# Kernel tuning notes

Hardware: AMD Instinct MI355X
Metric: run time of the kernel (lower is better)

Reference implementation:

```python
import jax, jax.numpy as jnp
import numpy as np

B, S, H = 2, 2048, 2048
NH, NKV, HD = 16, 4, 128
ROPE_BASE = 10000.0


def setup_inputs() -> dict:
    key = jax.random.key(0)
    ks = jax.random.split(key, 5)
    x = jax.random.normal(ks[0], (B, S, H), dtype=jnp.float32)
    position_ids = jnp.arange(S, dtype=jnp.int64 if jax.config.jax_enable_x64 else jnp.int32).reshape(1, S)
    # Linear weights stored as [in, out] (equivalent to torch weight.T)
    sc = 1.0 / np.sqrt(H)
    Wq = jax.random.normal(ks[1], (H, NH * HD), dtype=jnp.float32) * sc
    Wk = jax.random.normal(ks[2], (H, NKV * HD), dtype=jnp.float32) * sc
    Wv = jax.random.normal(ks[3], (H, NKV * HD), dtype=jnp.float32) * sc
    Wo = jax.random.normal(ks[4], (NH * HD, H), dtype=jnp.float32) * (1.0 / np.sqrt(NH * HD))
    return {"x": x, "position_ids": position_ids, "Wq": Wq, "Wk": Wk, "Wv": Wv, "Wo": Wo}


def _rope(q, k, position_ids):
    # q: [B,S,NH,HD], k: [B,S,NKV,HD]; Llama-style half-split RoPE
    half = HD // 2
    inv_freq = 1.0 / (ROPE_BASE ** (jnp.arange(0, half, dtype=jnp.float32) * 2.0 / HD))
    ang = position_ids.astype(jnp.float32)[..., None] * inv_freq  # [b,S,half]
    cos = jnp.concatenate([jnp.cos(ang), jnp.cos(ang)], axis=-1)[:, :, None, :]  # [b,S,1,HD]
    sin = jnp.concatenate([jnp.sin(ang), jnp.sin(ang)], axis=-1)[:, :, None, :]

    def rot_half(t):
        t1, t2 = t[..., :half], t[..., half:]
        return jnp.concatenate([-t2, t1], axis=-1)

    return q * cos + rot_half(q) * sin, k * cos + rot_half(k) * sin


def reference(x, position_ids, Wq, Wk, Wv, Wo):
    b, s, _ = x.shape
    q = (x @ Wq).reshape(b, s, NH, HD)
    k = (x @ Wk).reshape(b, s, NKV, HD)
    v = (x @ Wv).reshape(b, s, NKV, HD)
    q, k = _rope(q, k, position_ids)
    reps = NH // NKV
    k = jnp.repeat(k, reps, axis=2)  # repeat_interleave on head dim
    v = jnp.repeat(v, reps, axis=2)
    q = q.transpose(0, 2, 1, 3)  # [b,h,s,d]
    k = k.transpose(0, 2, 1, 3)
    v = v.transpose(0, 2, 1, 3)
    scores = jnp.einsum('bhqd,bhkd->bhqk', q, k) / jnp.sqrt(jnp.float32(HD))
    causal = jnp.triu(jnp.ones((s, s), dtype=bool), k=1)
    scores = jnp.where(causal, -jnp.inf, scores)
    attn = jax.nn.softmax(scores.astype(jnp.float32), axis=-1).astype(q.dtype)
    out = jnp.einsum('bhqk,bhkd->bhqd', attn, v)
    out = out.transpose(0, 2, 1, 3).reshape(b, s, NH * HD)
    return out @ Wo
```

## Files before the change

### kernel.cpp

```cpp
#include <hip/hip_runtime.h>
#include <stdint.h>

typedef unsigned short u16;
typedef __attribute__((ext_vector_type(8))) short short8;
typedef __attribute__((ext_vector_type(4))) float floatx4;

#define S_LEN 2048
#define NQKV 3072

#if __has_builtin(__builtin_amdgcn_exp2f)
#define EXP2F __builtin_amdgcn_exp2f
#else
#define EXP2F exp2f
#endif

__device__ inline float bf2f(u16 u) {
  union { uint32_t u; float f; } v; v.u = ((uint32_t)u) << 16; return v.f;
}
__device__ inline u16 f2bf(float f) {
  union { float f; uint32_t u; } v; v.f = f;
  uint32_t r = v.u + 0x7fffu + ((v.u >> 16) & 1u);
  return (u16)(r >> 16);
}
__device__ inline void gl2lds16(const u16* g, u16* l) {
  __builtin_amdgcn_global_load_lds((const __attribute__((address_space(1))) uint32_t*)g,
                                   (__attribute__((address_space(3))) uint32_t*)l, 16, 0, 0);
}

__global__ void cast_k(const float* __restrict__ in, u16* __restrict__ out, int n4) {
  int i = blockIdx.x * 256 + threadIdx.x;
  if (i >= n4) return;
  float4 v = ((const float4*)in)[i];
  ushort4 o;
  o.x = f2bf(v.x); o.y = f2bf(v.y); o.z = f2bf(v.z); o.w = f2bf(v.w);
  ((ushort4*)out)[i] = o;
}

__global__ void transpose_k(const float* __restrict__ in, u16* __restrict__ out, int K, int N) {
  __shared__ u16 tile[32][33];
  int n0 = blockIdx.x * 32, k0 = blockIdx.y * 32;
  int tx = threadIdx.x, ty = threadIdx.y;
#pragma unroll
  for (int i = 0; i < 4; i++)
    tile[ty + 8 * i][tx] = f2bf(in[(size_t)(k0 + ty + 8 * i) * N + n0 + tx]);
  __syncthreads();
#pragma unroll
  for (int i = 0; i < 4; i++)
    out[(size_t)(n0 + ty + 8 * i) * K + k0 + tx] = tile[tx][ty + 8 * i];
}

__global__ void vtrans_k(const u16* __restrict__ qkv, u16* __restrict__ vt) {
  __shared__ u16 tile[32][33];
  int bk = blockIdx.x * 32, bd = blockIdx.y * 32, bz = blockIdx.z;
  int bb = bz >> 2, kvh = bz & 3;
  const u16* src = qkv + ((size_t)bb * S_LEN) * NQKV + 2560 + kvh * 128;
  u16* dst = vt + (size_t)bz * 128 * 2048;
  int tx = threadIdx.x, ty = threadIdx.y;
#pragma unroll
  for (int i = 0; i < 4; i++)
    tile[ty + 8 * i][tx] = src[(size_t)(bk + ty + 8 * i) * NQKV + bd + tx];
  __syncthreads();
#pragma unroll
  for (int i = 0; i < 4; i++)
    dst[(size_t)(bd + ty + 8 * i) * 2048 + bk + tx] = tile[tx][ty + 8 * i];
}

template <bool OUTF32>
__global__ __launch_bounds__(256) void gemm_bt(const u16* __restrict__ A, const u16* __restrict__ Bt,
                                               void* __restrict__ Cv, int M, int N, int K) {
  __shared__ u16 As[128 * 32];
  __shared__ u16 Bs[128 * 32];
  const int m0 = blockIdx.y * 128, n0 = blockIdx.x * 128;
  const int t = threadIdx.x, w = t >> 6, lane = t & 63;
  const int quad = lane >> 4, l16 = lane & 15;
  const int wm = (w >> 1) * 64, wn = (w & 1) * 64;
  const int lrow = lane >> 2, lk = (lane & 3) * 8;
  floatx4 acc[4][4] = {};
  for (int k0 = 0; k0 < K; k0 += 32) {
#pragma unroll
    for (int c = 2 * w; c <= 2 * w + 1; ++c) {
      int row = c * 16 + lrow;
      gl2lds16(A + (size_t)(m0 + row) * K + k0 + lk, As + c * 512 + lane * 8);
      gl2lds16(Bt + (size_t)(n0 + row) * K + k0 + lk, Bs + c * 512 + lane * 8);
    }
    __syncthreads();
    short8 a[4], b[4];
#pragma unroll
    for (int mt = 0; mt < 4; mt++) a[mt] = *(const short8*)(As + (wm + mt * 16 + l16) * 32 + quad * 8);
#pragma unroll
    for (int nt = 0; nt < 4; nt++) b[nt] = *(const short8*)(Bs + (wn + nt * 16 + l16) * 32 + quad * 8);
#pragma unroll
    for (int mt = 0; mt < 4; mt++)
#pragma unroll
      for (int nt = 0; nt < 4; nt++)
        acc[mt][nt] = __builtin_amdgcn_mfma_f32_16x16x32_bf16(a[mt], b[nt], acc[mt][nt], 0, 0, 0);
    __syncthreads();
  }
#pragma unroll
  for (int mt = 0; mt < 4; mt++)
#pragma unroll
    for (int nt = 0; nt < 4; nt++)
#pragma unroll
      for (int r = 0; r < 4; r++) {
        int row = m0 + wm + mt * 16 + quad * 4 + r;
        int col = n0 + wn + nt * 16 + l16;
        if (OUTF32)
          ((float*)Cv)[(size_t)row * N + col] = acc[mt][nt][r];
        else
          ((u16*)Cv)[(size_t)row * N + col] = f2bf(acc[mt][nt][r]);
      }
}

__global__ __launch_bounds__(512, 2) void gemm256_k(const u16* __restrict__ A,
                                                    const u16* __restrict__ Bt,
                                                    u16* __restrict__ C, int N, int K) {
  __shared__ u16 Al[2][2][8192];
  __shared__ u16 Bl[2][2][8192];
  const int TN = N >> 8;
  int flat = blockIdx.x;
  const int cpx = gridDim.x >> 3;
  flat = (flat & 7) * cpx + (flat >> 3);
  const int m0 = (flat / TN) << 8, n0 = (flat % TN) << 8;
  const int t = threadIdx.x, w = t >> 6, lane = t & 63;
  const int quad = lane >> 4, l16 = lane & 15;
  const int wm = w >> 2, wn = w & 3;
  const int sr = t >> 3, sl = t & 7;
  floatx4 acc[2][2][4][2] = {};
  const int NKT = K >> 6;

  const int ra_l = wm * 64 + l16;
  const int rb_l = wn * 32 + l16;

#pragma unroll
  for (int round = 0; round < 2; round++) {
    int r = round * 64 + sr;
    int so = (sl ^ (r & 7)) << 3;
    gl2lds16(A + (size_t)(m0 + r) * K + so, &Al[0][0][0] + round * 4096 + t * 8);
    gl2lds16(Bt + (size_t)(n0 + r) * K + so, &Bl[0][0][0] + round * 4096 + t * 8);
    gl2lds16(Bt + (size_t)(n0 + 128 + r) * K + so, &Bl[0][1][0] + round * 4096 + t * 8);
    gl2lds16(A + (size_t)(m0 + 128 + r) * K + so, &Al[0][1][0] + round * 4096 + t * 8);
  }
  asm volatile("s_waitcnt vmcnt(0)" ::: "memory");
  __builtin_amdgcn_s_barrier();

  short8 af[4][2];
  short8 bf[2][2][2];

  for (int kt = 0; kt < NKT; kt++) {
    const int c = kt & 1;
    const u16* Ab = &Al[c][0][0];
    const u16* Bb = &Bl[c][0][0];
    u16* An = &Al[c ^ 1][0][0];
    u16* Bn = &Bl[c ^ 1][0][0];
    const int k1 = (kt + 1) << 6;
    const bool pf = (kt + 1 < NKT);
#pragma unroll
    for (int ph = 0; ph < 4; ph++) {
      const int mh = (ph >> 1);
      const int nh = (ph == 1 || ph == 2) ? 1 : 0;
      if (ph == 0 || ph == 2) {
#pragma unroll
        for (int mt = 0; mt < 4; mt++) {
          int ra = ra_l + mt * 16;
          const u16* base = Ab + mh * 8192 + ra * 64;
#pragma unroll
          for (int ks = 0; ks < 2; ks++)
            af[mt][ks] = *(const short8*)(base + (((ks * 4 + quad) ^ (ra & 7)) << 3));
        }
      }
      if (ph == 0 || ph == 1) {
#pragma unroll
        for (int nt = 0; nt < 2; nt++) {
          int rb = rb_l + nt * 16;
          const u16* base = Bb + nh * 8192 + rb * 64;
#pragma unroll
          for (int ks = 0; ks < 2; ks++)
            bf[nh][nt][ks] = *(const short8*)(base + (((ks * 4 + quad) ^ (rb & 7)) << 3));
        }
      }
      if (pf) {
        const u16* G;
        u16* L;
        int rbase;
        if (ph == 0)      { G = A;  L = An;        rbase = m0; }
        else if (ph == 1) { G = Bt; L = Bn;        rbase = n0; }
        else if (ph == 2) { G = Bt; L = Bn + 8192; rbase = n0 + 128; }
        else              { G = A;  L = An + 8192; rbase = m0 + 128; }
#pragma unroll
        for (int round = 0; round < 2; round++) {
          int r = round * 64 + sr;
          gl2lds16(G + (size_t)(rbase + r) * K + k1 + ((sl ^ (r & 7)) << 3),
                   L + round * 4096 + t * 8);
        }
      }
      __builtin_amdgcn_s_barrier();
      asm volatile("s_waitcnt lgkmcnt(0)" ::: "memory");
      __builtin_amdgcn_s_setprio(1);
#pragma unroll
      for (int mt = 0; mt < 4; mt++)
#pragma unroll
        for (int nt = 0; nt < 2; nt++)
#pragma unroll
          for (int ks = 0; ks < 2; ks++)
            acc[mh][nh][mt][nt] =
                __builtin_amdgcn_mfma_f32_16x16x32_bf16(af[mt][ks], bf[nh][nt][ks], acc[mh][nh][mt][nt], 0, 0, 0);
      __builtin_amdgcn_s_setprio(0);
      if (ph != 2) asm volatile("s_waitcnt vmcnt(4)" ::: "memory");
      __builtin_amdgcn_s_barrier();
    }
  }
#pragma unroll
  for (int mh = 0; mh < 2; mh++)
#pragma unroll
    for (int nh = 0; nh < 2; nh++)
#pragma unroll
      for (int mt = 0; mt < 4; mt++)
#pragma unroll
        for (int nt = 0; nt < 2; nt++)
#pragma unroll
          for (int r = 0; r < 4; r++) {
            int row = m0 + mh * 128 + wm * 64 + mt * 16 + quad * 4 + r;
            int col = n0 + nh * 128 + wn * 32 + nt * 16 + l16;
            C[(size_t)row * N + col] = f2bf(acc[mh][nh][mt][nt][r]);
          }
}

__global__ void rope_k(u16* __restrict__ qkv, const int* __restrict__ pos) {
  int idx = blockIdx.x * 256 + threadIdx.x;
  int i = idx & 63;
  int hh = (idx >> 6) % 20;
  int row = idx / (64 * 20);
  int s = row & (S_LEN - 1);
  float p = (float)pos[s];
  float freq = __expf(-(float)i * 0.015625f * 9.210340371976184f);
  float ang = p * freq;
  float c = cosf(ang), sn = sinf(ang);
  int col = (hh < 16) ? hh * 128 : 2048 + (hh - 16) * 128;
  size_t base = (size_t)row * NQKV + col + i;
  float t1 = bf2f(qkv[base]), t2 = bf2f(qkv[base + 64]);
  qkv[base] = f2bf(t1 * c - t2 * sn);
  qkv[base + 64] = f2bf(t2 * c + t1 * sn);
}

#define PL_LD 72
__global__ __launch_bounds__(256) void attn_k(const u16* __restrict__ qkv,
                                              const u16* __restrict__ vt,
                                              u16* __restrict__ ctx) {
  __shared__ u16 Kl[2][64 * 128];
  __shared__ u16 Vl[2][128 * 64];
  __shared__ u16 Pl[4][16 * PL_LD];
  const int p = blockIdx.x;
  const int h = blockIdx.y, bb = blockIdx.z;
  const int kvh = h >> 2;
  const int t = threadIdx.x, w = t >> 6, lane = t & 63;
  const int quad = lane >> 4, l16 = lane & 15;
  const int sx = l16 & 7;
  const int kkey0 = w * 16 + (lane >> 4);
  const int kslot = lane & 15;
  const int vd0 = w * 32 + (lane >> 3);
  const int vslot = lane & 7;
  const size_t rowbase = (size_t)bb * S_LEN;
  const u16* Kg0 = qkv + rowbase * NQKV + 2048 + kvh * 128;
  const u16* Vg0 = vt + (size_t)(bb * 4 + kvh) * 128 * 2048;
  const float c2 = 0.12751744f;
  short8 onesf = {16256, 16256, 16256, 16256, 16256, 16256, 16256, 16256};

  for (int phase = 0; phase < 2; phase++) {
    const int qt = phase ? p : 31 - p;
    const int rw = qt * 64 + w * 16;

    short8 qf[4];
#pragma unroll
    for (int ks = 0; ks < 4; ks++)
      qf[ks] = *(const short8*)(qkv + (rowbase + rw + l16) * NQKV + h * 128 + ks * 32 + quad * 8);

    floatx4 acc[8] = {};
    floatx4 accl = {0.f, 0.f, 0.f, 0.f};

    __syncthreads();
    {
      const u16* Kg = Kg0;
      const u16* Vg = Vg0;
#pragma unroll
      for (int ii = 0; ii < 4; ii++) {
        int key = kkey0 + ii * 4;
        gl2lds16(Kg + (size_t)key * NQKV + ((kslot ^ (key & 7)) * 8),
                 &Kl[0][0] + w * 2048 + ii * 512 + lane * 8);
      }
#pragma unroll
      for (int ii = 0; ii < 4; ii++) {
        int d = vd0 + ii * 8;
        gl2lds16(Vg + (size_t)d * 2048 + ((vslot ^ (d & 7)) * 8),
                 &Vl[0][0] + w * 2048 + ii * 512 + lane * 8);
      }
    }

    for (int kb = 0; kb <= qt; kb++) {
      const int cur = kb & 1;
      __syncthreads();
      if (kb < qt) {
        const u16* Kg = Kg0 + (size_t)(kb + 1) * 64 * NQKV;
        const u16* Vg = Vg0 + (kb + 1) * 64;
        u16* KlN = &Kl[cur ^ 1][0];
        u16* VlN = &Vl[cur ^ 1][0];
#pragma unroll
        for (int ii = 0; ii < 4; ii++) {
          int key = kkey0 + ii * 4;
          gl2lds16(Kg + (size_t)key * NQKV + ((kslot ^ (key & 7)) * 8),
                   KlN + w * 2048 + ii * 512 + lane * 8);
        }
#pragma unroll
        for (int ii = 0; ii < 4; ii++) {
          int d = vd0 + ii * 8;
          gl2lds16(Vg + (size_t)d * 2048 + ((vslot ^ (d & 7)) * 8),
                   VlN + w * 2048 + ii * 512 + lane * 8);
        }
      }
      const u16* KlB = &Kl[cur][0];
      const u16* VlB = &Vl[cur][0];

      floatx4 sc[4];
#pragma unroll
      for (int nt = 0; nt < 4; nt++) {
        const u16* Krow = KlB + (nt * 16 + l16) * 128;
        short8 kf[4];
#pragma unroll
        for (int ks = 0; ks < 4; ks++)
          kf[ks] = *(const short8*)(Krow + (((ks * 4 + quad) ^ sx) * 8));
        floatx4 s = {0.f, 0.f, 0.f, 0.f};
#pragma unroll
        for (int ks = 0; ks < 4; ks++) s = __builtin_amdgcn_mfma_f32_16x16x32_bf16(qf[ks], kf[ks], s, 0, 0, 0);
        sc[nt] = s;
      }
      const bool diag = (kb == qt);
#pragma unroll
      for (int nt = 0; nt < 4; nt++)
#pragma unroll
        for (int r = 0; r < 4; r++) {
          float e = EXP2F(sc[nt][r] * c2);
          if (diag) {
            int keyg = kb * 64 + nt * 16 + l16;
            int rowg = rw + quad * 4 + r;
            if (keyg > rowg) e = 0.f;
          }
          Pl[w][(quad * 4 + r) * PL_LD + nt * 16 + l16] = (u16)(__float_as_uint(e) >> 16);
        }
      short8 pf[2];
#pragma unroll
      for (int kh = 0; kh < 2; kh++)
        pf[kh] = *(const short8*)(&Pl[w][0] + l16 * PL_LD + kh * 32 + quad * 8);
      accl = __builtin_amdgcn_mfma_f32_16x16x32_bf16(pf[0], onesf, accl, 0, 0, 0);
      accl = __builtin_amdgcn_mfma_f32_16x16x32_bf16(pf[1], onesf, accl, 0, 0, 0);
#pragma unroll
      for (int nto = 0; nto < 8; nto++) {
        const u16* Vrow = VlB + (nto * 16 + l16) * 64;
        short8 vf0 = *(const short8*)(Vrow + ((quad ^ sx) * 8));
        short8 vf1 = *(const short8*)(Vrow + (((quad + 4) ^ sx) * 8));
        acc[nto] = __builtin_amdgcn_mfma_f32_16x16x32_bf16(pf[0], vf0, acc[nto], 0, 0, 0);
        acc[nto] = __builtin_amdgcn_mfma_f32_16x16x32_bf16(pf[1], vf1, acc[nto], 0, 0, 0);
      }
    }
#pragma unroll
    for (int r = 0; r < 4; r++) {
      float inv = 1.0f / accl[r];
      int rowg = rw + quad * 4 + r;
#pragma unroll
      for (int nto = 0; nto < 8; nto++) {
        int col = h * 128 + nto * 16 + l16;
        ctx[(rowbase + rowg) * 2048 + col] = f2bf(acc[nto][r] * inv);
      }
    }
  }
}

extern "C" void kernel_launch(void* const* d_in, const int* in_sizes, int n_in,
                              void* d_out, int out_size, void* d_ws, size_t ws_size,
                              hipStream_t stream) {
  const float* x  = (const float*)d_in[0];
  const int* pos  = (const int*)d_in[1];
  const float* Wq = (const float*)d_in[2];
  const float* Wk = (const float*)d_in[3];
  const float* Wv = (const float*)d_in[4];
  const float* Wo = (const float*)d_in[5];
  float* out = (float*)d_out;
  char* ws = (char*)d_ws;
  u16* Xb  = (u16*)(ws);
  u16* WT  = (u16*)(ws + 16777216);
  u16* WoT = (u16*)(ws + 29360128);
  u16* QKV = (u16*)(ws + 37748736);
  u16* CTX = (u16*)(ws + 62914560);
  u16* VT  = Xb;

  hipLaunchKernelGGL(cast_k, dim3(8192), dim3(256), 0, stream, x, Xb, 2097152);

  dim3 tb(32, 8);
  hipLaunchKernelGGL(transpose_k, dim3(64, 64), tb, 0, stream, Wq, WT, 2048, 2048);
  hipLaunchKernelGGL(transpose_k, dim3(16, 64), tb, 0, stream, Wk, WT + (size_t)2048 * 2048, 2048, 512);
  hipLaunchKernelGGL(transpose_k, dim3(16, 64), tb, 0, stream, Wv, WT + (size_t)2560 * 2048, 2048, 512);
  hipLaunchKernelGGL(transpose_k, dim3(64, 64), tb, 0, stream, Wo, WoT, 2048, 2048);

  hipLaunchKernelGGL(gemm256_k, dim3(192), dim3(512), 0, stream, Xb, WT, QKV, 3072, 2048);
  hipLaunchKernelGGL(rope_k, dim3(20480), dim3(256), 0, stream, QKV, pos);
  hipLaunchKernelGGL(vtrans_k, dim3(64, 4, 8), tb, 0, stream, QKV, VT);
  hipLaunchKernelGGL(attn_k, dim3(16, 16, 2), dim3(256), 0, stream, QKV, VT, CTX);
  hipLaunchKernelGGL(HIP_KERNEL_NAME(gemm_bt<true>), dim3(16, 32), dim3(256), 0, stream,
                     CTX, WoT, (void*)out, 4096, 2048, 2048);
}
```

Before: 308.7 us.

## Keep softmax probabilities in registers by transposing QK^T and permuting K rows

The QK^T MFMA now takes its operands in swapped order, producing transposed scores. K rows are loaded into LDS in a permuted key order so that each lane's score outputs already match the A-operand layout the P·V MFMA expects. The probabilities are packed into bf16 pairs in registers, which removes the LDS write/read round-trip through the Pl buffer and its shared-memory footprint. The causal mask index is rewritten for the new key permutation, and the row-sum and output indexing still rely on this permutation being consistent.

```diff
diff --git a/kernel.cpp b/kernel.cpp
--- a/kernel.cpp
+++ b/kernel.cpp
@@ -242,23 +242,21 @@
   qkv[base + 64] = f2bf(t2 * c + t1 * sn);
 }
 
-#define PL_LD 72
 __global__ __launch_bounds__(256) void attn_k(const u16* __restrict__ qkv,
                                               const u16* __restrict__ vt,
                                               u16* __restrict__ ctx) {
   __shared__ u16 Kl[2][64 * 128];
   __shared__ u16 Vl[2][128 * 64];
-  __shared__ u16 Pl[4][16 * PL_LD];
   const int p = blockIdx.x;
   const int h = blockIdx.y, bb = blockIdx.z;
   const int kvh = h >> 2;
   const int t = threadIdx.x, w = t >> 6, lane = t & 63;
   const int quad = lane >> 4, l16 = lane & 15;
   const int sx = l16 & 7;
-  const int kkey0 = w * 16 + (lane >> 4);
   const int kslot = lane & 15;
   const int vd0 = w * 32 + (lane >> 3);
   const int vslot = lane & 7;
+  const int grow0 = (w & 1) * 4 + (w >> 1) * 32 + quad;
   const size_t rowbase = (size_t)bb * S_LEN;
   const u16* Kg0 = qkv + rowbase * NQKV + 2048 + kvh * 128;
   const u16* Vg0 = vt + (size_t)(bb * 4 + kvh) * 128 * 2048;
@@ -268,6 +266,7 @@
   for (int phase = 0; phase < 2; phase++) {
     const int qt = phase ? p : 31 - p;
     const int rw = qt * 64 + w * 16;
+    const int qrow = rw + l16;
 
     short8 qf[4];
 #pragma unroll
@@ -283,8 +282,9 @@
       const u16* Vg = Vg0;
 #pragma unroll
       for (int ii = 0; ii < 4; ii++) {
-        int key = kkey0 + ii * 4;
-        gl2lds16(Kg + (size_t)key * NQKV + ((kslot ^ (key & 7)) * 8),
+        int p7 = (quad + 4 * ii) & 7;
+        int grow = grow0 + 8 * ii;
+        gl2lds16(Kg + (size_t)grow * NQKV + ((kslot ^ p7) * 8),
                  &Kl[0][0] + w * 2048 + ii * 512 + lane * 8);
       }
 #pragma unroll
@@ -305,8 +305,9 @@
         u16* VlN = &Vl[cur ^ 1][0];
 #pragma unroll
         for (int ii = 0; ii < 4; ii++) {
-          int key = kkey0 + ii * 4;
-          gl2lds16(Kg + (size_t)key * NQKV + ((kslot ^ (key & 7)) * 8),
+          int p7 = (quad + 4 * ii) & 7;
+          int grow = grow0 + 8 * ii;
+          gl2lds16(Kg + (size_t)grow * NQKV + ((kslot ^ p7) * 8),
                    KlN + w * 2048 + ii * 512 + lane * 8);
         }
 #pragma unroll
@@ -329,35 +330,44 @@
           kf[ks] = *(const short8*)(Krow + (((ks * 4 + quad) ^ sx) * 8));
         floatx4 s = {0.f, 0.f, 0.f, 0.f};
 #pragma unroll
-        for (int ks = 0; ks < 4; ks++) s = __builtin_amdgcn_mfma_f32_16x16x32_bf16(qf[ks], kf[ks], s, 0, 0, 0);
+        for (int ks = 0; ks < 4; ks++) s = __builtin_amdgcn_mfma_f32_16x16x32_bf16(kf[ks], qf[ks], s, 0, 0, 0);
         sc[nt] = s;
       }
       const bool diag = (kb == qt);
-#pragma unroll
-      for (int nt = 0; nt < 4; nt++)
+      uint32_t pw[8];
+#pragma unroll
+      for (int nt = 0; nt < 4; nt++) {
+        uint32_t w0 = 0, w1 = 0;
 #pragma unroll
         for (int r = 0; r < 4; r++) {
           float e = EXP2F(sc[nt][r] * c2);
           if (diag) {
-            int keyg = kb * 64 + nt * 16 + l16;
-            int rowg = rw + quad * 4 + r;
-            if (keyg > rowg) e = 0.f;
+            int keyg = kb * 64 + quad * 8 + (nt & 1) * 4 + (nt >> 1) * 32 + r;
+            if (keyg > qrow) e = 0.f;
           }
-          Pl[w][(quad * 4 + r) * PL_LD + nt * 16 + l16] = (u16)(__float_as_uint(e) >> 16);
-        }
-      short8 pf[2];
-#pragma unroll
-      for (int kh = 0; kh < 2; kh++)
-        pf[kh] = *(const short8*)(&Pl[w][0] + l16 * PL_LD + kh * 32 + quad * 8);
-      accl = __builtin_amdgcn_mfma_f32_16x16x32_bf16(pf[0], onesf, accl, 0, 0, 0);
-      accl = __builtin_amdgcn_mfma_f32_16x16x32_bf16(pf[1], onesf, accl, 0, 0, 0);
+          uint32_t b = __float_as_uint(e) >> 16;
+          if (r == 0) w0 = b;
+          else if (r == 1) w0 |= b << 16;
+          else if (r == 2) w1 = b;
+          else w1 |= b << 16;
+        }
+        pw[nt * 2] = w0;
+        pw[nt * 2 + 1] = w1;
+      }
+      union { short8 v; uint32_t u[4]; } pu0, pu1;
+      pu0.u[0] = pw[0]; pu0.u[1] = pw[1]; pu0.u[2] = pw[2]; pu0.u[3] = pw[3];
+      pu1.u[0] = pw[4]; pu1.u[1] = pw[5]; pu1.u[2] = pw[6]; pu1.u[3] = pw[7];
+      const short8 pf0 = pu0.v, pf1 = pu1.v;
+
+      accl = __builtin_amdgcn_mfma_f32_16x16x32_bf16(pf0, onesf, accl, 0, 0, 0);
+      accl = __builtin_amdgcn_mfma_f32_16x16x32_bf16(pf1, onesf, accl, 0, 0, 0);
 #pragma unroll
       for (int nto = 0; nto < 8; nto++) {
         const u16* Vrow = VlB + (nto * 16 + l16) * 64;
         short8 vf0 = *(const short8*)(Vrow + ((quad ^ sx) * 8));
         short8 vf1 = *(const short8*)(Vrow + (((quad + 4) ^ sx) * 8));
-        acc[nto] = __builtin_amdgcn_mfma_f32_16x16x32_bf16(pf[0], vf0, acc[nto], 0, 0, 0);
-        acc[nto] = __builtin_amdgcn_mfma_f32_16x16x32_bf16(pf[1], vf1, acc[nto], 0, 0, 0);
+        acc[nto] = __builtin_amdgcn_mfma_f32_16x16x32_bf16(pf0, vf0, acc[nto], 0, 0, 0);
+        acc[nto] = __builtin_amdgcn_mfma_f32_16x16x32_bf16(pf1, vf1, acc[nto], 0, 0, 0);
       }
     }
 #pragma unroll
```

Result: no change. 304.1 us (-1.5%).
